# Performance work log

Hardware: AMD Instinct MI355X
Metric: run time of the kernel (lower is better)

Reference implementation:

```python
import jax, jax.numpy as jnp
import numpy as np

B, N, C, H, D = 1, 256, 128, 4, 32  # batch, n_res, c_z, heads, head_dim
LN_EPS = 1e-5


def setup_inputs() -> dict:
    key = jax.random.key(0)
    ks = jax.random.split(key, 10)
    s = 0.02
    return {
        "act": jax.random.normal(ks[0], (B, N, N, C), dtype=jnp.float32),
        "mask": jnp.ones((B, N, N), dtype=jnp.float32),
        "ln_g": jnp.ones((C,), dtype=jnp.float32),
        "ln_b": jnp.zeros((C,), dtype=jnp.float32),
        "w2d": jax.random.normal(ks[1], (C, H), dtype=jnp.float32) * s,
        "wq": jax.random.normal(ks[2], (C, H, D), dtype=jnp.float32) * s,
        "wk": jax.random.normal(ks[3], (C, H, D), dtype=jnp.float32) * s,
        "wv": jax.random.normal(ks[4], (C, H, D), dtype=jnp.float32) * s,
        "wg": jax.random.normal(ks[5], (C, H, D), dtype=jnp.float32) * s,
        "bg": jnp.ones((H, D), dtype=jnp.float32),
        "wo": jax.random.normal(ks[6], (H, D, C), dtype=jnp.float32) * s,
        "bo": jnp.zeros((C,), dtype=jnp.float32),
    }


def reference(act, mask, ln_g, ln_b, w2d, wq, wk, wv, wg, bg, wo, bo):
    # LayerNorm over channel dim
    mu = jnp.mean(act, axis=-1, keepdims=True)
    var = jnp.mean(jnp.square(act - mu), axis=-1, keepdims=True)
    x = (act - mu) * jax.lax.rsqrt(var + LN_EPS) * ln_g + ln_b  # [B,N,N,C]

    # mask bias: [B, I, 1, 1, K]
    mask_bias = (1e9 * (mask - 1.0))[:, :, None, None, :]
    # nonbatched pair bias: [B, 1, H, Q, K]
    nb_bias = jnp.einsum('bqkc,ch->bhqk', x, w2d)[:, None]

    scale = 1.0 / jnp.sqrt(jnp.asarray(D, dtype=x.dtype))
    q = jnp.einsum('bijc,chd->bijhd', x, wq) * scale  # [B,I,Q,H,D]
    k = jnp.einsum('bijc,chd->bijhd', x, wk)
    v = jnp.einsum('bijc,chd->bijhd', x, wv)

    logits = jnp.einsum('biqhd,bikhd->bihqk', q, k) + mask_bias + nb_bias
    a = jax.nn.softmax(logits, axis=-1)  # [B,I,H,Q,K]
    o = jnp.einsum('bihqk,bikhd->biqhd', a, v)  # [B,I,Q,H,D]

    g = jax.nn.sigmoid(jnp.einsum('bijc,chd->bijhd', x, wg) + bg)
    o = o * g
    out = jnp.einsum('biqhd,hdc->biqc', o, wo) + bo  # [B,N,N,C]
    return out
```

## Files before the change

### kernel.cpp

```cpp
#include <hip/hip_runtime.h>

#define QK_SCALE 0.17677669529663689f

typedef float f4 __attribute__((ext_vector_type(4)));
typedef short bf16x8 __attribute__((ext_vector_type(8)));
typedef float f32x4 __attribute__((ext_vector_type(4)));
typedef unsigned short us4 __attribute__((ext_vector_type(4)));

__device__ __forceinline__ unsigned short f2bf(float x){
  unsigned int u = __float_as_uint(x);
  u += 0x7fffu + ((u >> 16) & 1u);
  return (unsigned short)(u >> 16);
}
__device__ __forceinline__ float bf2f(unsigned short h){
  return __uint_as_float(((unsigned int)h) << 16);
}
__device__ __forceinline__ f32x4 mfma16(bf16x8 a, bf16x8 b, f32x4 c){
  return __builtin_amdgcn_mfma_f32_16x16x32_bf16(a, b, c, 0, 0, 0);
}
__device__ __forceinline__ void gload_lds16(const void* g, void* s){
  __builtin_amdgcn_global_load_lds(
      (const __attribute__((address_space(1))) unsigned int*)g,
      (__attribute__((address_space(3))) unsigned int*)s, 16, 0, 0);
}

__global__ __launch_bounds__(256)
void k_prep(const float* __restrict__ wq, const float* __restrict__ wk,
            const float* __restrict__ wv, const float* __restrict__ wg,
            const float* __restrict__ wo, unsigned short* __restrict__ pk)
{
  const int m = blockIdx.x;
  const float* W = (m==0)? wq : (m==1)? wk : (m==2)? wv : (m==3)? wg : wo;
  const float scale = (m==0)? QK_SCALE : 1.0f;
  unsigned short* dst = pk + (long)m * 32768;
  for (int ent = threadIdx.x; ent < 2048; ent += 256){
    const int l = ent & 63, ktn = ent >> 6;
    const int kt = ktn & 3, nt = ktn >> 2;
    unsigned short* ph = dst + ((nt*4 + kt)*2 + 0)*512 + l*8;
    unsigned short* pl = dst + ((nt*4 + kt)*2 + 1)*512 + l*8;
    #pragma unroll
    for (int e = 0; e < 8; ++e){
      const int row = kt*32 + (l>>4)*8 + e;
      const int col = nt*16 + (l&15);
      float v = W[row*128 + col] * scale;
      unsigned short hh = f2bf(v);
      ph[e] = hh;
      pl[e] = f2bf(v - bf2f(hh));
    }
  }
}

__global__ __launch_bounds__(512, 4)
void k_proj(const float* __restrict__ act, const float* __restrict__ ln_g,
            const float* __restrict__ ln_b, const float* __restrict__ w2d,
            const unsigned short* __restrict__ pk, const float* __restrict__ bg,
            unsigned short* __restrict__ qf, unsigned short* __restrict__ kf,
            unsigned short* __restrict__ vt, unsigned short* __restrict__ gg,
            float* __restrict__ b2d)
{
  __shared__ unsigned short afr[8*4*2*512];
  __shared__ unsigned short sc[4*640];
  const int t = threadIdx.x, w = t>>6, l = t&63, g16 = l>>4, c = l&15;
  const long p0 = (long)blockIdx.x * 128;
  const int bi = (int)(p0 >> 8);
  const int qb0 = (int)(p0 & 255);
  const int row = w*16 + c;

  {
    const float* ap = act + (p0 + row)*128;
    f4 xv[4][2];
    #pragma unroll
    for (int kt = 0; kt < 4; ++kt){
      xv[kt][0] = *(const f4*)(ap + kt*32 + g16*8);
      xv[kt][1] = *(const f4*)(ap + kt*32 + g16*8 + 4);
    }
    float s = 0.f, s2 = 0.f;
    #pragma unroll
    for (int kt = 0; kt < 4; ++kt)
      #pragma unroll
      for (int u = 0; u < 2; ++u)
        #pragma unroll
        for (int e = 0; e < 4; ++e){
          float x = xv[kt][u][e]; s += x; s2 += x*x;
        }
    s += __shfl_xor(s,16); s2 += __shfl_xor(s2,16);
    s += __shfl_xor(s,32); s2 += __shfl_xor(s2,32);
    const float mu = s*(1.f/128.f);
    const float iv = rsqrtf(fmaxf(s2*(1.f/128.f)-mu*mu,0.f)+1e-5f);

    float pb0=0.f, pb1=0.f, pb2=0.f, pb3=0.f;
    #pragma unroll
    for (int kt = 0; kt < 4; ++kt){
      bf16x8 hv, lv;
      #pragma unroll
      for (int u = 0; u < 2; ++u){
        const int cb = kt*32 + g16*8 + u*4;
        f4 lg = *(const f4*)(ln_g + cb);
        f4 lb = *(const f4*)(ln_b + cb);
        #pragma unroll
        for (int e0 = 0; e0 < 4; ++e0){
          float vv = (xv[kt][u][e0]-mu)*iv*lg[e0] + lb[e0];
          f4 wp = *(const f4*)(w2d + (cb+e0)*4);
          pb0 += vv*wp[0]; pb1 += vv*wp[1]; pb2 += vv*wp[2]; pb3 += vv*wp[3];
          unsigned short hh = f2bf(vv);
          hv[u*4+e0] = (short)hh;
          lv[u*4+e0] = (short)f2bf(vv - bf2f(hh));
        }
      }
      *(bf16x8*)&afr[((w*4+kt)*2+0)*512 + l*8] = hv;
      *(bf16x8*)&afr[((w*4+kt)*2+1)*512 + l*8] = lv;
    }
    pb0 += __shfl_xor(pb0,16); pb1 += __shfl_xor(pb1,16);
    pb2 += __shfl_xor(pb2,16); pb3 += __shfl_xor(pb3,16);
    pb0 += __shfl_xor(pb0,32); pb1 += __shfl_xor(pb1,32);
    pb2 += __shfl_xor(pb2,32); pb3 += __shfl_xor(pb3,32);
    const float pbsel = (g16==0)? pb0 : (g16==1)? pb1 : (g16==2)? pb2 : pb3;
    b2d[g16*65536 + (int)p0 + row] = pbsel;
  }
  __syncthreads();

  #pragma unroll
  for (int pass = 0; pass < 2; ++pass){
    bf16x8 bh0[4], bl0[4], bh1[4], bl1[4];
    { const int ntg = w*4 + pass*2;
      #pragma unroll
      for (int kt = 0; kt < 4; ++kt){
        bh0[kt] = *(const bf16x8*)(pk + ((ntg*4+kt)*2+0)*512 + l*8);
        bl0[kt] = *(const bf16x8*)(pk + ((ntg*4+kt)*2+1)*512 + l*8);
        bh1[kt] = *(const bf16x8*)(pk + (((ntg+1)*4+kt)*2+0)*512 + l*8);
        bl1[kt] = *(const bf16x8*)(pk + (((ntg+1)*4+kt)*2+1)*512 + l*8);
      } }
    for (int rt = 0; rt < 8; ++rt){
      bf16x8 ah[4], al[4];
      #pragma unroll
      for (int kt = 0; kt < 4; ++kt){
        ah[kt] = *(const bf16x8*)&afr[((rt*4+kt)*2+0)*512 + l*8];
        al[kt] = *(const bf16x8*)&afr[((rt*4+kt)*2+1)*512 + l*8];
      }
      f32x4 a0 = {0.f,0.f,0.f,0.f}, a1 = {0.f,0.f,0.f,0.f};
      #pragma unroll
      for (int kt = 0; kt < 4; ++kt){
        a0 = mfma16(ah[kt], bh0[kt], a0);
        a1 = mfma16(ah[kt], bh1[kt], a1);
        a0 = mfma16(ah[kt], bl0[kt], a0);
        a1 = mfma16(ah[kt], bl1[kt], a1);
        a0 = mfma16(al[kt], bh0[kt], a0);
        a1 = mfma16(al[kt], bh1[kt], a1);
      }
      if (w < 4){
        unsigned short* scw = sc + w*640;
        #pragma unroll
        for (int j = 0; j < 4; ++j){
          scw[(g16*4+j)*40 + c]      = f2bf(a0[j]);
          scw[(g16*4+j)*40 + 16 + c] = f2bf(a1[j]);
        }
        asm volatile("" ::: "memory");
        bf16x8 fr = *(const bf16x8*)&scw[c*40 + g16*8];
        const int head = (w&1)*2 + pass;
        unsigned short* dst = (w < 2) ? qf : kf;
        *(bf16x8*)&dst[(((long)bi*4+head)*16 + (qb0>>4) + rt)*512 + l*8] = fr;
        asm volatile("" ::: "memory");
      } else if (w < 6){
        const int ntv0 = (w-4)*4 + pass*2;
        const int kv = qb0 + rt*16 + g16*4;
        #pragma unroll
        for (int np = 0; np < 2; ++np){
          const int colg = (ntv0+np)*16 + c;
          const int head = colg >> 5, d = colg & 31;
          f32x4 aa = np ? a1 : a0;
          us4 v4;
          #pragma unroll
          for (int j = 0; j < 4; ++j) v4[j] = f2bf(aa[j]);
          const int vb = (d*512 + kv*2) ^ ((d&7)<<4);
          *(us4*)((char*)vt + ((long)bi*4+head)*16384 + vb) = v4;
        }
      } else {
        const int colb = (w-6)*64 + pass*32;
        const int row0 = (int)p0 + rt*16 + g16*4;
        const float bg0 = bg[colb + c];
        const float bg1 = bg[colb + 16 + c];
        #pragma unroll
        for (int j = 0; j < 4; ++j){
          float g0 = 1.f/(1.f + __expf(-(a0[j] + bg0)));
          float g1 = 1.f/(1.f + __expf(-(a1[j] + bg1)));
          gg[(row0+j)*128 + colb + c]      = f2bf(g0);
          gg[(row0+j)*128 + colb + 16 + c] = f2bf(g1);
        }
      }
    }
  }
}

__global__ __launch_bounds__(256, 3)
void k_attn(const unsigned short* __restrict__ qf, const unsigned short* __restrict__ kfg,
            const unsigned short* __restrict__ vt, const unsigned short* __restrict__ gg,
            const float* __restrict__ b2d, const float* __restrict__ mask,
            unsigned short* __restrict__ obf)
{
  __shared__ unsigned short k_s[16*512];
  __shared__ unsigned short v_s[8192];
  __shared__ unsigned short p_s[4*2112];
  __shared__ float mb_s[256];
  const int t = threadIdx.x, w = t>>6, l = t&63, g16 = l>>4, c = l&15;
  const int bi = blockIdx.x >> 2, h = blockIdx.x & 3;
  const int base = (bi*4+h)*8192;

  #pragma unroll
  for (int cc = 0; cc < 8; ++cc){
    const int ch = w*8 + cc;
    if (ch < 16) gload_lds16(kfg + base + ch*512 + l*8, k_s + ch*512);
    else         gload_lds16(vt + base + (ch-16)*512 + l*8, v_s + (ch-16)*512);
  }
  mb_s[t] = 1e9f * (mask[bi*256 + t] - 1.0f);
  asm volatile("s_waitcnt vmcnt(0)" ::: "memory");
  __syncthreads();

  unsigned short* pw = p_s + w*2112;

  for (int im = 0; im < 4; ++im){
    const int q0 = w*64 + im*16;
    const bf16x8 qfr = *(const bf16x8*)(qf + base + (q0>>4)*512 + l*8);
    f32x4 sa[16];
    const float* bq = b2d + h*65536 + (q0 + g16*4)*256;
    #pragma unroll
    for (int nt = 0; nt < 16; ++nt){
      const int kcol = nt*16 + c;
      const float mbv = mb_s[kcol];
      f32x4 ci;
      ci[0]=mbv+bq[kcol];     ci[1]=mbv+bq[256+kcol];
      ci[2]=mbv+bq[512+kcol]; ci[3]=mbv+bq[768+kcol];
      sa[nt] = ci;
    }
    #pragma unroll
    for (int nt = 0; nt < 16; ++nt)
      sa[nt] = mfma16(qfr, *(const bf16x8*)(k_s + nt*512 + l*8), sa[nt]);
    float mx0=-3e38f,mx1=-3e38f,mx2=-3e38f,mx3=-3e38f;
    #pragma unroll
    for (int nt = 0; nt < 16; ++nt){
      mx0 = fmaxf(mx0, sa[nt][0]); mx1 = fmaxf(mx1, sa[nt][1]);
      mx2 = fmaxf(mx2, sa[nt][2]); mx3 = fmaxf(mx3, sa[nt][3]);
    }
    #pragma unroll
    for (int d = 1; d < 16; d <<= 1){
      mx0 = fmaxf(mx0, __shfl_xor(mx0, d)); mx1 = fmaxf(mx1, __shfl_xor(mx1, d));
      mx2 = fmaxf(mx2, __shfl_xor(mx2, d)); mx3 = fmaxf(mx3, __shfl_xor(mx3, d));
    }
    float s0=0.f, s1=0.f, s2=0.f, s3=0.f;
    #pragma unroll
    for (int nt = 0; nt < 16; ++nt){
      float e0 = __expf(sa[nt][0]-mx0), e1 = __expf(sa[nt][1]-mx1);
      float e2 = __expf(sa[nt][2]-mx2), e3 = __expf(sa[nt][3]-mx3);
      s0 += e0; s1 += e1; s2 += e2; s3 += e3;
      sa[nt][0]=e0; sa[nt][1]=e1; sa[nt][2]=e2; sa[nt][3]=e3;
    }
    #pragma unroll
    for (int d = 1; d < 16; d <<= 1){
      s0 += __shfl_xor(s0, d); s1 += __shfl_xor(s1, d);
      s2 += __shfl_xor(s2, d); s3 += __shfl_xor(s3, d);
    }
    float invs[4] = {1.f/s0, 1.f/s1, 1.f/s2, 1.f/s3};
    f32x4 oa0 = {0.f,0.f,0.f,0.f}, oa1 = {0.f,0.f,0.f,0.f};
    #pragma unroll
    for (int ph = 0; ph < 2; ++ph){
      #pragma unroll
      for (int n8 = 0; n8 < 8; ++n8){
        const int nt = ph*8 + n8;
        const int cb = n8*16 + c;
        pw[(g16*4+0)*132 + cb] = f2bf(sa[nt][0]);
        pw[(g16*4+1)*132 + cb] = f2bf(sa[nt][1]);
        pw[(g16*4+2)*132 + cb] = f2bf(sa[nt][2]);
        pw[(g16*4+3)*132 + cb] = f2bf(sa[nt][3]);
      }
      asm volatile("s_waitcnt lgkmcnt(0)" ::: "memory");
      __builtin_amdgcn_sched_barrier(0);
      #pragma unroll
      for (int ktl = 0; ktl < 4; ++ktl){
        const int kt = ph*4 + ktl;
        bf16x8 pf = *(const bf16x8*)(pw + c*132 + ktl*32 + g16*8);
        const int vb0 = ((c*512      + kt*64 + g16*16) ^ ((c&7)<<4));
        const int vb1 = (((16+c)*512 + kt*64 + g16*16) ^ ((c&7)<<4));
        oa0 = mfma16(pf, *(const bf16x8*)((const char*)v_s + vb0), oa0);
        oa1 = mfma16(pf, *(const bf16x8*)((const char*)v_s + vb1), oa1);
      }
      asm volatile("" ::: "memory");
      __builtin_amdgcn_sched_barrier(0);
    }
    const int row0 = bi*256 + q0 + g16*4;
    #pragma unroll
    for (int j = 0; j < 4; ++j){
      float gv0 = bf2f(gg[(row0+j)*128 + h*32 + c]);
      float gv1 = bf2f(gg[(row0+j)*128 + h*32 + 16 + c]);
      obf[(row0+j)*128 + h*32 + c]      = f2bf(oa0[j]*invs[j]*gv0);
      obf[(row0+j)*128 + h*32 + 16 + c] = f2bf(oa1[j]*invs[j]*gv1);
    }
  }
}

__global__ __launch_bounds__(512, 4)
void k_out(const unsigned short* __restrict__ obf, const unsigned short* __restrict__ pko,
           const float* __restrict__ bo, float* __restrict__ out)
{
  __shared__ unsigned short afr[32*512];
  const int t = threadIdx.x, w = t>>6, l = t&63, g16 = l>>4, c = l&15;
  const long p0 = (long)blockIdx.x * 128;

  #pragma unroll
  for (int u = 0; u < 4; ++u){
    const int pr = w*4 + u;
    const int rt = pr >> 2, kt = pr & 3;
    gload_lds16(obf + (p0 + rt*16 + c)*128 + kt*32 + g16*8, afr + pr*512);
  }
  asm volatile("s_waitcnt vmcnt(0)" ::: "memory");
  __syncthreads();

  bf16x8 bh[4], bl[4];
  #pragma unroll
  for (int kt = 0; kt < 4; ++kt){
    bh[kt] = *(const bf16x8*)(pko + ((w*4+kt)*2+0)*512 + l*8);
    bl[kt] = *(const bf16x8*)(pko + ((w*4+kt)*2+1)*512 + l*8);
  }
  const float bov = bo[w*16 + c];
  for (int rt = 0; rt < 8; ++rt){
    f32x4 a0 = {bov, bov, bov, bov};
    #pragma unroll
    for (int kt = 0; kt < 4; ++kt){
      bf16x8 af = *(const bf16x8*)&afr[(rt*4+kt)*512 + l*8];
      a0 = mfma16(af, bh[kt], a0);
      a0 = mfma16(af, bl[kt], a0);
    }
    const int row0 = (int)p0 + rt*16 + g16*4;
    #pragma unroll
    for (int j = 0; j < 4; ++j)
      out[(row0+j)*128 + w*16 + c] = a0[j];
  }
}

extern "C" void kernel_launch(void* const* d_in, const int* in_sizes, int n_in,
                              void* d_out, int out_size, void* d_ws, size_t ws_size,
                              hipStream_t stream) {
  const float* act  = (const float*)d_in[0];
  const float* mask = (const float*)d_in[1];
  const float* ln_g = (const float*)d_in[2];
  const float* ln_b = (const float*)d_in[3];
  const float* w2d  = (const float*)d_in[4];
  const float* wq   = (const float*)d_in[5];
  const float* wk   = (const float*)d_in[6];
  const float* wv   = (const float*)d_in[7];
  const float* wg   = (const float*)d_in[8];
  const float* bg   = (const float*)d_in[9];
  const float* wo   = (const float*)d_in[10];
  const float* bo   = (const float*)d_in[11];
  float* out = (float*)d_out;

  char* ws = (char*)d_ws;
  unsigned short* qf  = (unsigned short*)(ws);
  unsigned short* kfb = (unsigned short*)(ws + 16777216L);
  unsigned short* vt  = (unsigned short*)(ws + 33554432L);
  unsigned short* gg  = (unsigned short*)(ws + 50331648L);
  unsigned short* obf = (unsigned short*)(ws + 67108864L);
  float* b2d = (float*)(ws + 83886080L);
  unsigned short* pk = (unsigned short*)(ws + 84934656L);

  k_prep<<<5, 256, 0, stream>>>(wq, wk, wv, wg, wo, pk);
  k_proj<<<512, 512, 0, stream>>>(act, ln_g, ln_b, w2d, pk, bg,
                                  qf, kfb, vt, gg, b2d);
  k_attn<<<1024, 256, 0, stream>>>(qf, kfb, vt, gg, b2d, mask, obf);
  k_out<<<512, 512, 0, stream>>>(obf, pk + 4*32768, bo, out);
}
```

Before: 108.3 us.

## Transpose MFMA operands in attention so each lane owns a query row

The attention kernel swaps the A/B operands of both MFMAs, so each lane's accumulator holds four consecutive keys or output channels for a single query row instead of four rows. Bias and gate loads, P stores and output stores become 4-wide vectors, and the softmax reductions drop from 4-register, 4-step shuffles to one register with 2 steps. The P scratch buffer loses its row padding and uses an XOR swizzle instead, and exp is computed as exp2 with a folded log2e FMA. The risk is bank conflicts in the new swizzled layout and a different register schedule.

```diff
diff --git a/kernel.cpp b/kernel.cpp
--- a/kernel.cpp
+++ b/kernel.cpp
@@ -199,7 +199,7 @@
 {
   __shared__ unsigned short k_s[16*512];
   __shared__ unsigned short v_s[8192];
-  __shared__ unsigned short p_s[4*2112];
+  __shared__ unsigned short p_s[4*2048];
   __shared__ float mb_s[256];
   const int t = threadIdx.x, w = t>>6, l = t&63, g16 = l>>4, c = l&15;
   const int bi = blockIdx.x >> 2, h = blockIdx.x & 3;
@@ -215,84 +215,77 @@
   asm volatile("s_waitcnt vmcnt(0)" ::: "memory");
   __syncthreads();
 
-  unsigned short* pw = p_s + w*2112;
+  char* pw = (char*)(p_s + w*2048);
+  const int swz = (c&7)<<4;
 
   for (int im = 0; im < 4; ++im){
     const int q0 = w*64 + im*16;
     const bf16x8 qfr = *(const bf16x8*)(qf + base + (q0>>4)*512 + l*8);
+    const float* bq = b2d + h*65536 + (q0 + c)*256 + g16*4;
     f32x4 sa[16];
-    const float* bq = b2d + h*65536 + (q0 + g16*4)*256;
     #pragma unroll
     for (int nt = 0; nt < 16; ++nt){
-      const int kcol = nt*16 + c;
-      const float mbv = mb_s[kcol];
+      f4 bv = *(const f4*)(bq + nt*16);
+      f4 mv = *(const f4*)&mb_s[nt*16 + g16*4];
       f32x4 ci;
-      ci[0]=mbv+bq[kcol];     ci[1]=mbv+bq[256+kcol];
-      ci[2]=mbv+bq[512+kcol]; ci[3]=mbv+bq[768+kcol];
-      sa[nt] = ci;
-    }
-    #pragma unroll
-    for (int nt = 0; nt < 16; ++nt)
-      sa[nt] = mfma16(qfr, *(const bf16x8*)(k_s + nt*512 + l*8), sa[nt]);
-    float mx0=-3e38f,mx1=-3e38f,mx2=-3e38f,mx3=-3e38f;
+      ci[0]=bv[0]+mv[0]; ci[1]=bv[1]+mv[1]; ci[2]=bv[2]+mv[2]; ci[3]=bv[3]+mv[3];
+      sa[nt] = mfma16(*(const bf16x8*)(k_s + nt*512 + l*8), qfr, ci);
+    }
+    float mx = fmaxf(fmaxf(sa[0][0], sa[0][1]), fmaxf(sa[0][2], sa[0][3]));
+    #pragma unroll
+    for (int nt = 1; nt < 16; ++nt)
+      mx = fmaxf(mx, fmaxf(fmaxf(sa[nt][0], sa[nt][1]), fmaxf(sa[nt][2], sa[nt][3])));
+    mx = fmaxf(mx, __shfl_xor(mx, 16));
+    mx = fmaxf(mx, __shfl_xor(mx, 32));
+    const float nmx = -mx * 1.44269504f;
+    float sum = 0.f;
     #pragma unroll
     for (int nt = 0; nt < 16; ++nt){
-      mx0 = fmaxf(mx0, sa[nt][0]); mx1 = fmaxf(mx1, sa[nt][1]);
-      mx2 = fmaxf(mx2, sa[nt][2]); mx3 = fmaxf(mx3, sa[nt][3]);
-    }
-    #pragma unroll
-    for (int d = 1; d < 16; d <<= 1){
-      mx0 = fmaxf(mx0, __shfl_xor(mx0, d)); mx1 = fmaxf(mx1, __shfl_xor(mx1, d));
-      mx2 = fmaxf(mx2, __shfl_xor(mx2, d)); mx3 = fmaxf(mx3, __shfl_xor(mx3, d));
-    }
-    float s0=0.f, s1=0.f, s2=0.f, s3=0.f;
-    #pragma unroll
-    for (int nt = 0; nt < 16; ++nt){
-      float e0 = __expf(sa[nt][0]-mx0), e1 = __expf(sa[nt][1]-mx1);
-      float e2 = __expf(sa[nt][2]-mx2), e3 = __expf(sa[nt][3]-mx3);
-      s0 += e0; s1 += e1; s2 += e2; s3 += e3;
-      sa[nt][0]=e0; sa[nt][1]=e1; sa[nt][2]=e2; sa[nt][3]=e3;
-    }
-    #pragma unroll
-    for (int d = 1; d < 16; d <<= 1){
-      s0 += __shfl_xor(s0, d); s1 += __shfl_xor(s1, d);
-      s2 += __shfl_xor(s2, d); s3 += __shfl_xor(s3, d);
-    }
-    float invs[4] = {1.f/s0, 1.f/s1, 1.f/s2, 1.f/s3};
+      #pragma unroll
+      for (int j = 0; j < 4; ++j){
+        float e = exp2f(fmaf(sa[nt][j], 1.44269504f, nmx));
+        sa[nt][j] = e; sum += e;
+      }
+    }
+    sum += __shfl_xor(sum, 16);
+    sum += __shfl_xor(sum, 32);
+    const float inv = 1.f / sum;
     f32x4 oa0 = {0.f,0.f,0.f,0.f}, oa1 = {0.f,0.f,0.f,0.f};
     #pragma unroll
-    for (int ph = 0; ph < 2; ++ph){
-      #pragma unroll
-      for (int n8 = 0; n8 < 8; ++n8){
-        const int nt = ph*8 + n8;
-        const int cb = n8*16 + c;
-        pw[(g16*4+0)*132 + cb] = f2bf(sa[nt][0]);
-        pw[(g16*4+1)*132 + cb] = f2bf(sa[nt][1]);
-        pw[(g16*4+2)*132 + cb] = f2bf(sa[nt][2]);
-        pw[(g16*4+3)*132 + cb] = f2bf(sa[nt][3]);
+    for (int ph2 = 0; ph2 < 2; ++ph2){
+      #pragma unroll
+      for (int ntl = 0; ntl < 8; ++ntl){
+        const int nt = ph2*8 + ntl;
+        us4 pk4;
+        pk4[0] = f2bf(sa[nt][0]); pk4[1] = f2bf(sa[nt][1]);
+        pk4[2] = f2bf(sa[nt][2]); pk4[3] = f2bf(sa[nt][3]);
+        *(us4*)(pw + c*256 + ((ntl*32 + g16*8) ^ swz)) = pk4;
       }
       asm volatile("s_waitcnt lgkmcnt(0)" ::: "memory");
       __builtin_amdgcn_sched_barrier(0);
       #pragma unroll
       for (int ktl = 0; ktl < 4; ++ktl){
-        const int kt = ph*4 + ktl;
-        bf16x8 pf = *(const bf16x8*)(pw + c*132 + ktl*32 + g16*8);
-        const int vb0 = ((c*512      + kt*64 + g16*16) ^ ((c&7)<<4));
-        const int vb1 = (((16+c)*512 + kt*64 + g16*16) ^ ((c&7)<<4));
-        oa0 = mfma16(pf, *(const bf16x8*)((const char*)v_s + vb0), oa0);
-        oa1 = mfma16(pf, *(const bf16x8*)((const char*)v_s + vb1), oa1);
+        const int kt = ph2*4 + ktl;
+        bf16x8 pf = *(const bf16x8*)(pw + c*256 + ((ktl*64 + g16*16) ^ swz));
+        const int vb0 = ((c*512      + kt*64 + g16*16) ^ swz);
+        const int vb1 = (((16+c)*512 + kt*64 + g16*16) ^ swz);
+        oa0 = mfma16(*(const bf16x8*)((const char*)v_s + vb0), pf, oa0);
+        oa1 = mfma16(*(const bf16x8*)((const char*)v_s + vb1), pf, oa1);
       }
       asm volatile("" ::: "memory");
       __builtin_amdgcn_sched_barrier(0);
     }
-    const int row0 = bi*256 + q0 + g16*4;
+    const int row = bi*256 + q0 + c;
+    us4 gv0 = *(const us4*)&gg[row*128 + h*32 + g16*4];
+    us4 gv1 = *(const us4*)&gg[row*128 + h*32 + 16 + g16*4];
+    us4 o0, o1;
     #pragma unroll
     for (int j = 0; j < 4; ++j){
-      float gv0 = bf2f(gg[(row0+j)*128 + h*32 + c]);
-      float gv1 = bf2f(gg[(row0+j)*128 + h*32 + 16 + c]);
-      obf[(row0+j)*128 + h*32 + c]      = f2bf(oa0[j]*invs[j]*gv0);
-      obf[(row0+j)*128 + h*32 + 16 + c] = f2bf(oa1[j]*invs[j]*gv1);
-    }
+      o0[j] = f2bf(oa0[j] * inv * bf2f(gv0[j]));
+      o1[j] = f2bf(oa1[j] * inv * bf2f(gv1[j]));
+    }
+    *(us4*)&obf[row*128 + h*32 + g16*4]      = o0;
+    *(us4*)&obf[row*128 + h*32 + 16 + g16*4] = o1;
   }
 }
 
```

Measured after the change: 110.1 us. Within noise of the previous version (+1.6%).
